# Optimization experiments

Hardware: AMD Instinct MI355X
Metric: run time of the kernel (lower is better)

## Reference

```python
import jax, jax.numpy as jnp
import numpy as np

GROUPS = 32
EPS = 1e-5


def setup_inputs() -> dict:
    key = jax.random.key(0)
    ks = jax.random.split(key, 4)
    B, C, H, W = 4, 256, 64, 64
    x = jax.random.normal(ks[0], (B, C, H, W), dtype=jnp.float32)
    gn_w = jnp.ones((C,), jnp.float32)
    gn_b = jnp.zeros((C,), jnp.float32)
    qkv_w = jax.random.normal(ks[1], (3 * C, C), dtype=jnp.float32) * (C ** -0.5)
    qkv_b = jnp.zeros((3 * C,), jnp.float32)
    proj_w = jax.random.normal(ks[2], (C, C), dtype=jnp.float32) * (C ** -0.5)
    proj_b = jnp.zeros((C,), jnp.float32)
    return {"x": x, "gn_w": gn_w, "gn_b": gn_b, "qkv_w": qkv_w,
            "qkv_b": qkv_b, "proj_w": proj_w, "proj_b": proj_b}


def _group_norm(x, w, b):
    B, C, H, W = x.shape
    xr = x.reshape(B, GROUPS, -1)                      # [B, G, (C/G)*H*W]
    mean = xr.mean(axis=-1, keepdims=True)
    var = xr.var(axis=-1, keepdims=True)               # biased, like torch
    h = ((xr - mean) * jax.lax.rsqrt(var + EPS)).reshape(B, C, H, W)
    return h * w[None, :, None, None] + b[None, :, None, None]


def reference(x, gn_w, gn_b, qkv_w, qkv_b, proj_w, proj_b):
    B, C, H, W = x.shape
    h = _group_norm(x, gn_w, gn_b)
    # 1x1 conv == channel GEMM
    qkv = jnp.einsum('oc,bchw->bohw', qkv_w, h) + qkv_b[None, :, None, None]
    qkv = qkv.reshape(B, 3, C, H * W)
    q, k, v = qkv[:, 0], qkv[:, 1], qkv[:, 2]          # [B, C, N]
    scale = C ** (-0.5)
    attn = jax.nn.softmax(jnp.einsum('bci,bcj->bij', q, k) * scale, axis=-1)
    out = jnp.einsum('bij,bcj->bci', attn, v).reshape(B, C, H, W)
    out = jnp.einsum('oc,bchw->bohw', proj_w, out) + proj_b[None, :, None, None]
    return x + out
```

## Files before the change

### kernel.cpp

```cpp
#include <hip/hip_runtime.h>
#include <hip/hip_bf16.h>
#include <math.h>

typedef __bf16 bf16;
typedef __bf16 bf16x8 __attribute__((ext_vector_type(8)));
typedef __bf16 bf16x4 __attribute__((ext_vector_type(4)));
typedef float f32x4 __attribute__((ext_vector_type(4)));
typedef float f32x16 __attribute__((ext_vector_type(16)));

#define MFMA16(a, b, c) __builtin_amdgcn_mfma_f32_16x16x32_bf16(a, b, c, 0, 0, 0)
#define MFMA32(a, b, c) __builtin_amdgcn_mfma_f32_32x32x16_bf16(a, b, c, 0, 0, 0)

#define SCALEK 0.09016844005555896f

typedef const __attribute__((address_space(1))) void* gas_t;
typedef __attribute__((address_space(3))) void* las_t;

__global__ __launch_bounds__(256) void wcvt_kernel(const float* __restrict__ qw,
                                                   bf16* __restrict__ qwb) {
  int t = blockIdx.x * 256 + threadIdx.x;
  float4 v = *(const float4*)(qw + (size_t)t * 4);
  bf16x4 o;
  o[0] = (bf16)v.x; o[1] = (bf16)v.y; o[2] = (bf16)v.z; o[3] = (bf16)v.w;
  *(bf16x4*)(qwb + (size_t)t * 4) = o;
}

__global__ __launch_bounds__(256) void gn_kernel(
    const float* __restrict__ x, const float* __restrict__ gw,
    const float* __restrict__ gb, bf16* __restrict__ h) {
  const int bg = blockIdx.x;
  const int b = bg >> 5, g = bg & 31;
  const size_t base = (size_t)(b * 256 + g * 8) * 4096;
  const float* xp = x + base;
  bf16* hp = h + base;
  const int tid = threadIdx.x;

  float s = 0.f, ss = 0.f;
  for (int i = tid * 4; i < 32768; i += 1024) {
    float4 v = *(const float4*)(xp + i);
    s += v.x + v.y + v.z + v.w;
    ss += v.x * v.x + v.y * v.y + v.z * v.z + v.w * v.w;
  }
#pragma unroll
  for (int off = 32; off; off >>= 1) {
    s += __shfl_down(s, off);
    ss += __shfl_down(ss, off);
  }
  __shared__ float red[8];
  if ((tid & 63) == 0) {
    red[(tid >> 6) * 2] = s;
    red[(tid >> 6) * 2 + 1] = ss;
  }
  __syncthreads();
  s = red[0] + red[2] + red[4] + red[6];
  ss = red[1] + red[3] + red[5] + red[7];
  const float mean = s * (1.f / 32768.f);
  const float var = ss * (1.f / 32768.f) - mean * mean;
  const float rstd = rsqrtf(var + 1e-5f);

  for (int i = tid * 4; i < 32768; i += 1024) {
    float4 v = *(const float4*)(xp + i);
    int c = g * 8 + (i >> 12);
    float a = gw[c] * rstd;
    float b2 = gb[c] - mean * a;
    bf16x4 o;
    o[0] = (bf16)(v.x * a + b2);
    o[1] = (bf16)(v.y * a + b2);
    o[2] = (bf16)(v.z * a + b2);
    o[3] = (bf16)(v.w * a + b2);
    *(bf16x4*)(hp + i) = o;
  }
}

__global__ __launch_bounds__(256) void qkv_gemm(
    const bf16* __restrict__ h, const bf16* __restrict__ wb,
    const float* __restrict__ bias, bf16* __restrict__ qt,
    bf16* __restrict__ kt, bf16* __restrict__ vcm) {
  const int b = blockIdx.z;
  const int o0 = blockIdx.y * 64;
  const int p0 = blockIdx.x * 64;
  __shared__ bf16 Alds[2][64][32];
  __shared__ bf16 Blds[2][64][56];
  const int tid = threadIdx.x;
  const int lane = tid & 63, wid = tid >> 6;
  const int lr = lane & 15, lg = lane >> 4;
  const int wm = wid >> 1, wn = wid & 1;
  const bf16* hb = h + (size_t)b * 256 * 4096;

  const int arow = tid >> 2, ac8 = (tid & 3) * 8;
  const int bcc = tid >> 3, bp8 = (tid & 7) * 8;

#define QKV_STAGE_A(K0, BUF)                                                  \
  __builtin_amdgcn_global_load_lds(                                           \
      (gas_t)(const void*)(wb + (size_t)(o0 + arow) * 256 + (K0) + ac8),      \
      (las_t)(void*)(&Alds[BUF][0][0] + tid * 8), 16, 0, 0);

  f32x4 acc[2][2] = {};

  QKV_STAGE_A(0, 0);
  {
    bf16x8 v = *(const bf16x8*)(hb + (size_t)bcc * 4096 + p0 + bp8);
#pragma unroll
    for (int e = 0; e < 8; ++e) Blds[0][bp8 + e][bcc] = v[e];
  }
  __syncthreads();

  for (int k = 0; k < 8; ++k) {
    const int cur = k & 1, nb = cur ^ 1;
    if (k < 7) {
      QKV_STAGE_A((k + 1) * 32, nb);
      bf16x8 v =
          *(const bf16x8*)(hb + (size_t)((k + 1) * 32 + bcc) * 4096 + p0 + bp8);
#pragma unroll
      for (int e = 0; e < 8; ++e) Blds[nb][bp8 + e][bcc] = v[e];
    }
    bf16x8 af[2], bfr[2];
#pragma unroll
    for (int mi = 0; mi < 2; ++mi)
      af[mi] = *(const bf16x8*)&Alds[cur][wm * 32 + mi * 16 + lr][lg * 8];
#pragma unroll
    for (int ni = 0; ni < 2; ++ni)
      bfr[ni] = *(const bf16x8*)&Blds[cur][wn * 32 + ni * 16 + lr][lg * 8];
#pragma unroll
    for (int mi = 0; mi < 2; ++mi)
#pragma unroll
      for (int ni = 0; ni < 2; ++ni)
        acc[mi][ni] = MFMA16(af[mi], bfr[ni], acc[mi][ni]);
    __syncthreads();
  }
#undef QKV_STAGE_A

#pragma unroll
  for (int mi = 0; mi < 2; ++mi) {
#pragma unroll
    for (int ni = 0; ni < 2; ++ni) {
#pragma unroll
      for (int r = 0; r < 4; ++r) {
        int o = o0 + wm * 32 + mi * 16 + lg * 4 + r;
        int p = p0 + wn * 32 + ni * 16 + lr;
        float val = acc[mi][ni][r] + bias[o];
        if (o < 256) {
          qt[((size_t)b * 4096 + p) * 256 + o] = (bf16)val;
        } else if (o < 512) {
          kt[((size_t)b * 4096 + p) * 256 + (o - 256)] = (bf16)(val * SCALEK);
        } else {
          vcm[((size_t)b * 256 + (o - 512)) * 4096 + p] = (bf16)val;
        }
      }
    }
  }
}

template <int S>
__global__ __launch_bounds__(256, 2) void flash_attn(
    const bf16* __restrict__ qt, const bf16* __restrict__ kt,
    const bf16* __restrict__ vcm, bf16* __restrict__ Opart,
    float* __restrict__ l_g) {
  constexpr int NCOMBO = 4 * S;
  constexpr int CSH = (S == 4) ? 4 : (S == 2) ? 3 : 2;
  constexpr int NIT = (4096 / S) / 32;
  const int bid = blockIdx.x;
  const int combo = bid & (NCOMBO - 1);
  const int qtile = bid >> CSH;
  const int b = combo & 3;
  const int split = combo >> 2;
  const int i0 = qtile * 128;
  const int jbase = split * (4096 / S);

  __shared__ bf16 Klds[2][32][256];
  __shared__ bf16 Vlds[2][256][32];
  const int tid = threadIdx.x;
  const int lane = tid & 63, w = tid >> 6;
  const int ln = lane & 31;
  const int hv = lane >> 5;
  const bf16* qb = qt + (size_t)b * 4096 * 256;
  const bf16* kb = kt + (size_t)b * 4096 * 256;
  const bf16* vb = vcm + (size_t)b * 256 * 4096;

  const int qrow = i0 + w * 32 + ln;
  bf16x8 qf[16];
#pragma unroll
  for (int ks = 0; ks < 16; ++ks)
    qf[ks] = *(const bf16x8*)(qb + (size_t)qrow * 256 + ks * 16 + hv * 8);

  int koff[4], voff[4];
#pragma unroll
  for (int it = 0; it < 4; ++it) {
    int chunk = tid + 256 * it;
    int krow = chunk >> 5;
    koff[it] = krow * 256 + ((((chunk & 31) ^ (krow & 7)) * 8));
    int vrow = chunk >> 2;
    voff[it] = vrow * 4096 + (((chunk & 3) ^ ((vrow >> 2) & 3)) * 8);
  }

#define STAGE_K(JT, BUF)                                                      \
  {                                                                           \
    const int j0s = jbase + (JT) * 32;                                        \
    _Pragma("unroll") for (int it = 0; it < 4; ++it) {                        \
      int chunk = tid + 256 * it;                                             \
      __builtin_amdgcn_global_load_lds(                                       \
          (gas_t)(const void*)(kb + (size_t)j0s * 256 + koff[it]),            \
          (las_t)(void*)(&Klds[BUF][0][0] + chunk * 8), 16, 0, 0);            \
    }                                                                         \
  }
#define STAGE_V(JT, BUF)                                                      \
  {                                                                           \
    const int j0s = jbase + (JT) * 32;                                        \
    _Pragma("unroll") for (int it = 0; it < 4; ++it) {                        \
      int chunk = tid + 256 * it;                                             \
      __builtin_amdgcn_global_load_lds(                                       \
          (gas_t)(const void*)(vb + (size_t)j0s + voff[it]),                  \
          (las_t)(void*)(&Vlds[BUF][0][0] + chunk * 8), 16, 0, 0);            \
    }                                                                         \
  }

  float llane = 0.f;
  f32x16 accO[8] = {};
  const int kswz = ln & 7;
  const int vswz = (ln >> 2) & 3;

  STAGE_K(0, 0);
  STAGE_V(0, 0);
  asm volatile("s_waitcnt vmcnt(0)" ::: "memory");
  __builtin_amdgcn_s_barrier();

  f32x16 a0 = {}, a1 = {};
#pragma unroll
  for (int ks = 0; ks < 8; ++ks) {
    bf16x8 kf0 = *(const bf16x8*)&Klds[0][ln][((2 * ks + hv) ^ kswz) * 8];
    bf16x8 kf1 =
        *(const bf16x8*)&Klds[0][ln][((2 * (ks + 8) + hv) ^ kswz) * 8];
    a0 = MFMA32(kf0, qf[ks], a0);
    a1 = MFMA32(kf1, qf[ks + 8], a1);
  }
  STAGE_K(1, 1);

  for (int t = 0; t < NIT; ++t) {
    asm volatile("s_waitcnt vmcnt(0)" ::: "memory");
    __builtin_amdgcn_s_barrier();

    if (t + 1 < NIT) STAGE_V(t + 1, (t + 1) & 1);
    if (t + 2 < NIT) STAGE_K(t + 2, t & 1);

    float pv[16];
#pragma unroll
    for (int r = 0; r < 16; ++r) pv[r] = exp2f(a0[r] + a1[r]);
    llane += (((pv[0] + pv[1]) + (pv[2] + pv[3])) +
              ((pv[4] + pv[5]) + (pv[6] + pv[7]))) +
             (((pv[8] + pv[9]) + (pv[10] + pv[11])) +
              ((pv[12] + pv[13]) + (pv[14] + pv[15])));

    int pk[8];
#pragma unroll
    for (int q4 = 0; q4 < 8; ++q4)
      asm("v_cvt_pk_bf16_f32 %0, %1, %2"
          : "=v"(pk[q4])
          : "v"(pv[q4 * 2]), "v"(pv[q4 * 2 + 1]));
    bf16x8 pfrag[2];
#pragma unroll
    for (int s = 0; s < 2; ++s) {
      int xa = pk[s * 4 + 0], ya = pk[s * 4 + 2];
      int xb = pk[s * 4 + 1], yb = pk[s * 4 + 3];
      asm("v_permlane32_swap_b32 %0, %1" : "+v"(xa), "+v"(ya));
      asm("v_permlane32_swap_b32 %0, %1" : "+v"(xb), "+v"(yb));
      union { int i[4]; bf16x8 v; } u;
      u.i[0] = xa; u.i[1] = xb; u.i[2] = ya; u.i[3] = yb;
      pfrag[s] = u.v;
    }

    const bf16(*Kc)[256] = Klds[(t + 1) & 1];
    const bf16(*Vc)[32] = Vlds[t & 1];
    __builtin_amdgcn_s_setprio(1);
    if (t + 1 < NIT) {
      f32x16 n0 = {}, n1 = {};
#pragma unroll
      for (int u = 0; u < 8; ++u) {
        bf16x8 kf0 = *(const bf16x8*)&Kc[ln][((2 * u + hv) ^ kswz) * 8];
        n0 = MFMA32(kf0, qf[u], n0);
        bf16x8 kf1 =
            *(const bf16x8*)&Kc[ln][((2 * (u + 8) + hv) ^ kswz) * 8];
        n1 = MFMA32(kf1, qf[u + 8], n1);
        bf16x8 vf0 = *(const bf16x8*)&Vc[u * 32 + ln][((hv) ^ vswz) * 8];
        accO[u] = MFMA32(vf0, pfrag[0], accO[u]);
        bf16x8 vf1 = *(const bf16x8*)&Vc[u * 32 + ln][((2 + hv) ^ vswz) * 8];
        accO[u] = MFMA32(vf1, pfrag[1], accO[u]);
      }
      a0 = n0;
      a1 = n1;
    } else {
#pragma unroll
      for (int u = 0; u < 8; ++u) {
        bf16x8 vf0 = *(const bf16x8*)&Vc[u * 32 + ln][((hv) ^ vswz) * 8];
        accO[u] = MFMA32(vf0, pfrag[0], accO[u]);
        bf16x8 vf1 = *(const bf16x8*)&Vc[u * 32 + ln][((2 + hv) ^ vswz) * 8];
        accO[u] = MFMA32(vf1, pfrag[1], accO[u]);
      }
    }
    __builtin_amdgcn_s_setprio(0);
  }
#undef STAGE_K
#undef STAGE_V

  bf16* ob = Opart + ((size_t)(split * 4 + b) * 4096 + qrow) * 256;
#pragma unroll
  for (int cb = 0; cb < 8; ++cb) {
#pragma unroll
    for (int g = 0; g < 4; ++g) {
      int lo, hi;
      asm("v_cvt_pk_bf16_f32 %0, %1, %2"
          : "=v"(lo)
          : "v"(accO[cb][g * 4 + 0]), "v"(accO[cb][g * 4 + 1]));
      asm("v_cvt_pk_bf16_f32 %0, %1, %2"
          : "=v"(hi)
          : "v"(accO[cb][g * 4 + 2]), "v"(accO[cb][g * 4 + 3]));
      int2 val; val.x = lo; val.y = hi;
      *(int2*)(ob + cb * 32 + g * 8 + hv * 4) = val;
    }
  }
  {
    int xa = __float_as_int(llane);
    int ya = xa;
    asm("v_permlane32_swap_b32 %0, %1" : "+v"(xa), "+v"(ya));
    float ltot = __int_as_float(xa) + __int_as_float(ya);
    if (hv == 0)
      l_g[(size_t)(split * 4 + b) * 4096 + qrow] = ltot;
  }
}

template <int S>
__global__ __launch_bounds__(256) void proj_fused(
    const bf16* __restrict__ Opart, const float* __restrict__ l_g,
    const float* __restrict__ w, const float* __restrict__ bias,
    const float* __restrict__ x, float* __restrict__ out) {
  const int b = blockIdx.y;
  const int p0 = blockIdx.x * 64;
  __shared__ bf16 Wlds[256][32];
  __shared__ bf16 Blds[64][32];
  __shared__ float Linv[64];
  const int tid = threadIdx.x;
  const int lane = tid & 63, wid = tid >> 6;
  const int lr = lane & 15, lg = lane >> 4;

  if (tid < 64) {
    float L = 0.f;
#pragma unroll
    for (int s = 0; s < S; ++s)
      L += l_g[(size_t)(s * 4 + b) * 4096 + p0 + tid];
    Linv[tid] = 1.f / L;
  }
  __syncthreads();

  const int pr = tid >> 2, c8b = (tid & 3) * 8;
  const float invp = Linv[pr];

  float4 wreg[4][2];
  bf16x8 breg[S];

#define PROJ_READ(K0)                                                         \
  {                                                                           \
    _Pragma("unroll") for (int it = 0; it < 4; ++it) {                        \
      int chunk = tid + 256 * it;                                             \
      int row = chunk >> 2, c8 = (chunk & 3) * 8;                             \
      const float* src = w + (size_t)row * 256 + (K0) + c8;                   \
      wreg[it][0] = *(const float4*)src;                                      \
      wreg[it][1] = *(const float4*)(src + 4);                                \
    }                                                                         \
    _Pragma("unroll") for (int s = 0; s < S; ++s) breg[s] =                   \
        *(const bf16x8*)(Opart +                                              \
                         ((size_t)(s * 4 + b) * 4096 + p0 + pr) * 256 +       \
                         (K0) + c8b);                                         \
  }
#define PROJ_WRITE()                                                          \
  {                                                                           \
    _Pragma("unroll") for (int it = 0; it < 4; ++it) {                        \
      int chunk = tid + 256 * it;                                             \
      int row = chunk >> 2, c8 = (chunk & 3) * 8;                             \
      bf16x8 bv;                                                              \
      bv[0] = (bf16)wreg[it][0].x; bv[1] = (bf16)wreg[it][0].y;               \
      bv[2] = (bf16)wreg[it][0].z; bv[3] = (bf16)wreg[it][0].w;               \
      bv[4] = (bf16)wreg[it][1].x; bv[5] = (bf16)wreg[it][1].y;               \
      bv[6] = (bf16)wreg[it][1].z; bv[7] = (bf16)wreg[it][1].w;               \
      *(bf16x8*)&Wlds[row][c8] = bv;                                          \
    }                                                                         \
    {                                                                         \
      float a8[8] = {};                                                       \
      _Pragma("unroll") for (int s = 0; s < S; ++s) {                         \
        _Pragma("unroll") for (int e = 0; e < 8; ++e) a8[e] +=                \
            (float)breg[s][e];                                                \
      }                                                                       \
      bf16x8 bv;                                                              \
      _Pragma("unroll") for (int e = 0; e < 8; ++e) bv[e] =                   \
          (bf16)(a8[e] * invp);                                               \
      *(bf16x8*)&Blds[pr][c8b] = bv;                                          \
    }                                                                         \
  }

  f32x4 acc[4][4] = {};

  PROJ_READ(0);
  PROJ_WRITE();
  __syncthreads();

  for (int k = 0; k < 8; ++k) {
    if (k < 7) PROJ_READ((k + 1) * 32);

    bf16x8 af[4], bfr[4];
#pragma unroll
    for (int mi = 0; mi < 4; ++mi)
      af[mi] = *(const bf16x8*)&Wlds[wid * 64 + mi * 16 + lr][lg * 8];
#pragma unroll
    for (int ni = 0; ni < 4; ++ni)
      bfr[ni] = *(const bf16x8*)&Blds[ni * 16 + lr][lg * 8];
#pragma unroll
    for (int mi = 0; mi < 4; ++mi)
#pragma unroll
      for (int ni = 0; ni < 4; ++ni)
        acc[mi][ni] = MFMA16(af[mi], bfr[ni], acc[mi][ni]);

    __syncthreads();
    if (k < 7) {
      PROJ_WRITE();
      __syncthreads();
    }
  }
#undef PROJ_READ
#undef PROJ_WRITE

#pragma unroll
  for (int mi = 0; mi < 4; ++mi) {
#pragma unroll
    for (int ni = 0; ni < 4; ++ni) {
#pragma unroll
      for (int r = 0; r < 4; ++r) {
        int o = wid * 64 + mi * 16 + lg * 4 + r;
        int p = p0 + ni * 16 + lr;
        size_t idx = ((size_t)b * 256 + o) * 4096 + p;
        out[idx] = acc[mi][ni][r] + bias[o] + x[idx];
      }
    }
  }
}

extern "C" void kernel_launch(void* const* d_in, const int* in_sizes, int n_in,
                              void* d_out, int out_size, void* d_ws,
                              size_t ws_size, hipStream_t stream) {
  (void)in_sizes; (void)n_in; (void)out_size;
  const float* x = (const float*)d_in[0];
  const float* gn_w = (const float*)d_in[1];
  const float* gn_b = (const float*)d_in[2];
  const float* qkv_w = (const float*)d_in[3];
  const float* qkv_b = (const float*)d_in[4];
  const float* proj_w = (const float*)d_in[5];
  const float* proj_b = (const float*)d_in[6];
  float* out = (float*)d_out;

  const size_t MB = 1024ull * 1024ull;
  char* ws = (char*)d_ws;
  bf16* h = (bf16*)(ws);
  bf16* qt = (bf16*)(ws + 8 * MB);
  bf16* kt = (bf16*)(ws + 16 * MB);
  bf16* vcm = (bf16*)(ws + 24 * MB);

  int S;
  if (ws_size >= 32 * MB + 4 * 8 * MB + 4ull * 16384 * sizeof(float)) S = 4;
  else if (ws_size >= 32 * MB + 2 * 8 * MB + 2ull * 16384 * sizeof(float)) S = 2;
  else S = 1;

  bf16* Opart;
  float* l_g;
  bf16* qwb;
  if (S >= 2) {
    Opart = (bf16*)(ws + 32 * MB);
    l_g = (float*)(ws + 32 * MB + (size_t)S * 8 * MB);
    qwb = Opart;
  } else {
    Opart = h;
    l_g = (float*)(ws + 32 * MB);
    qwb = (bf16*)(ws + 32 * MB + 256 * 1024);
  }

  wcvt_kernel<<<192, 256, 0, stream>>>(qkv_w, qwb);
  gn_kernel<<<128, 256, 0, stream>>>(x, gn_w, gn_b, h);
  qkv_gemm<<<dim3(64, 12, 4), 256, 0, stream>>>(h, qwb, qkv_b, qt, kt, vcm);
  if (S == 4) {
    flash_attn<4><<<32 * 16, 256, 0, stream>>>(qt, kt, vcm, Opart, l_g);
    proj_fused<4><<<dim3(64, 4), 256, 0, stream>>>(Opart, l_g, proj_w, proj_b,
                                                   x, out);
  } else if (S == 2) {
    flash_attn<2><<<32 * 8, 256, 0, stream>>>(qt, kt, vcm, Opart, l_g);
    proj_fused<2><<<dim3(64, 4), 256, 0, stream>>>(Opart, l_g, proj_w, proj_b,
                                                   x, out);
  } else {
    flash_attn<1><<<32 * 4, 256, 0, stream>>>(qt, kt, vcm, Opart, l_g);
    proj_fused<1><<<dim3(64, 4), 256, 0, stream>>>(Opart, l_g, proj_w, proj_b,
                                                   x, out);
  }
}
```

Measured before the change: 180.1 us.

## Process two query row groups per wave with 4-stage K/V pipeline

```diff
diff --git a/kernel.cpp b/kernel.cpp
--- a/kernel.cpp
+++ b/kernel.cpp
@@ -152,7 +152,7 @@
 }
 
 template <int S>
-__global__ __launch_bounds__(256, 2) void flash_attn(
+__global__ __launch_bounds__(256, 1) void flash_attn(
     const bf16* __restrict__ qt, const bf16* __restrict__ kt,
     const bf16* __restrict__ vcm, bf16* __restrict__ Opart,
     float* __restrict__ l_g) {
@@ -164,11 +164,11 @@
   const int qtile = bid >> CSH;
   const int b = combo & 3;
   const int split = combo >> 2;
-  const int i0 = qtile * 128;
+  const int i0 = qtile * 256;
   const int jbase = split * (4096 / S);
 
-  __shared__ bf16 Klds[2][32][256];
-  __shared__ bf16 Vlds[2][256][32];
+  __shared__ bf16 Klds[4][32][256];
+  __shared__ bf16 Vlds[4][256][32];
   const int tid = threadIdx.x;
   const int lane = tid & 63, w = tid >> 6;
   const int ln = lane & 31;
@@ -177,11 +177,14 @@
   const bf16* kb = kt + (size_t)b * 4096 * 256;
   const bf16* vb = vcm + (size_t)b * 256 * 4096;
 
-  const int qrow = i0 + w * 32 + ln;
-  bf16x8 qf[16];
-#pragma unroll
-  for (int ks = 0; ks < 16; ++ks)
-    qf[ks] = *(const bf16x8*)(qb + (size_t)qrow * 256 + ks * 16 + hv * 8);
+  const int qrow0 = i0 + w * 64 + ln;
+  const int qrow1 = qrow0 + 32;
+  bf16x8 qf0[16], qf1[16];
+#pragma unroll
+  for (int ks = 0; ks < 16; ++ks) {
+    qf0[ks] = *(const bf16x8*)(qb + (size_t)qrow0 * 256 + ks * 16 + hv * 8);
+    qf1[ks] = *(const bf16x8*)(qb + (size_t)qrow1 * 256 + ks * 16 + hv * 8);
+  }
 
   int koff[4], voff[4];
 #pragma unroll
@@ -193,7 +196,7 @@
     voff[it] = vrow * 4096 + (((chunk & 3) ^ ((vrow >> 2) & 3)) * 8);
   }
 
-#define STAGE_K(JT, BUF)                                                      \
+#define STAGE(JT, BUF)                                                        \
   {                                                                           \
     const int j0s = jbase + (JT) * 32;                                        \
     _Pragma("unroll") for (int it = 0; it < 4; ++it) {                        \
@@ -201,130 +204,116 @@
       __builtin_amdgcn_global_load_lds(                                       \
           (gas_t)(const void*)(kb + (size_t)j0s * 256 + koff[it]),            \
           (las_t)(void*)(&Klds[BUF][0][0] + chunk * 8), 16, 0, 0);            \
-    }                                                                         \
-  }
-#define STAGE_V(JT, BUF)                                                      \
-  {                                                                           \
-    const int j0s = jbase + (JT) * 32;                                        \
-    _Pragma("unroll") for (int it = 0; it < 4; ++it) {                        \
-      int chunk = tid + 256 * it;                                             \
       __builtin_amdgcn_global_load_lds(                                       \
           (gas_t)(const void*)(vb + (size_t)j0s + voff[it]),                  \
           (las_t)(void*)(&Vlds[BUF][0][0] + chunk * 8), 16, 0, 0);            \
     }                                                                         \
   }
 
-  float llane = 0.f;
-  f32x16 accO[8] = {};
+#define SOFTPACK(A0, A1, LL, PF)                                              \
+  {                                                                           \
+    float pv[16];                                                             \
+    _Pragma("unroll") for (int r = 0; r < 16; ++r) pv[r] =                    \
+        exp2f((A0)[r] + (A1)[r]);                                             \
+    (LL) += (((pv[0] + pv[1]) + (pv[2] + pv[3])) +                            \
+             ((pv[4] + pv[5]) + (pv[6] + pv[7]))) +                           \
+            (((pv[8] + pv[9]) + (pv[10] + pv[11])) +                          \
+             ((pv[12] + pv[13]) + (pv[14] + pv[15])));                        \
+    int pk[8];                                                                \
+    _Pragma("unroll") for (int q4 = 0; q4 < 8; ++q4)                          \
+        asm("v_cvt_pk_bf16_f32 %0, %1, %2"                                    \
+            : "=v"(pk[q4])                                                    \
+            : "v"(pv[q4 * 2]), "v"(pv[q4 * 2 + 1]));                          \
+    _Pragma("unroll") for (int s = 0; s < 2; ++s) {                           \
+      int xa = pk[s * 4 + 0], ya = pk[s * 4 + 2];                             \
+      int xb = pk[s * 4 + 1], yb = pk[s * 4 + 3];                             \
+      asm("v_permlane32_swap_b32 %0, %1" : "+v"(xa), "+v"(ya));               \
+      asm("v_permlane32_swap_b32 %0, %1" : "+v"(xb), "+v"(yb));               \
+      union { int i[4]; bf16x8 v; } u;                                        \
+      u.i[0] = xa; u.i[1] = xb; u.i[2] = ya; u.i[3] = yb;                     \
+      (PF)[s] = u.v;                                                          \
+    }                                                                         \
+  }
+
+  float ll0 = 0.f, ll1 = 0.f;
+  f32x16 acc0[8] = {}, acc1[8] = {};
   const int kswz = ln & 7;
   const int vswz = (ln >> 2) & 3;
 
-  STAGE_K(0, 0);
-  STAGE_V(0, 0);
-  asm volatile("s_waitcnt vmcnt(0)" ::: "memory");
-  __builtin_amdgcn_s_barrier();
-
-  f32x16 a0 = {}, a1 = {};
-#pragma unroll
-  for (int ks = 0; ks < 8; ++ks) {
-    bf16x8 kf0 = *(const bf16x8*)&Klds[0][ln][((2 * ks + hv) ^ kswz) * 8];
-    bf16x8 kf1 =
-        *(const bf16x8*)&Klds[0][ln][((2 * (ks + 8) + hv) ^ kswz) * 8];
-    a0 = MFMA32(kf0, qf[ks], a0);
-    a1 = MFMA32(kf1, qf[ks + 8], a1);
-  }
-  STAGE_K(1, 1);
+  STAGE(0, 0);
+  STAGE(1, 1);
+  STAGE(2, 2);
 
   for (int t = 0; t < NIT; ++t) {
-    asm volatile("s_waitcnt vmcnt(0)" ::: "memory");
+    if (t + 2 < NIT)
+      asm volatile("s_waitcnt vmcnt(16)" ::: "memory");
+    else if (t + 1 < NIT)
+      asm volatile("s_waitcnt vmcnt(8)" ::: "memory");
+    else
+      asm volatile("s_waitcnt vmcnt(0)" ::: "memory");
     __builtin_amdgcn_s_barrier();
-
-    if (t + 1 < NIT) STAGE_V(t + 1, (t + 1) & 1);
-    if (t + 2 < NIT) STAGE_K(t + 2, t & 1);
-
-    float pv[16];
-#pragma unroll
-    for (int r = 0; r < 16; ++r) pv[r] = exp2f(a0[r] + a1[r]);
-    llane += (((pv[0] + pv[1]) + (pv[2] + pv[3])) +
-              ((pv[4] + pv[5]) + (pv[6] + pv[7]))) +
-             (((pv[8] + pv[9]) + (pv[10] + pv[11])) +
-              ((pv[12] + pv[13]) + (pv[14] + pv[15])));
-
-    int pk[8];
-#pragma unroll
-    for (int q4 = 0; q4 < 8; ++q4)
-      asm("v_cvt_pk_bf16_f32 %0, %1, %2"
-          : "=v"(pk[q4])
-          : "v"(pv[q4 * 2]), "v"(pv[q4 * 2 + 1]));
-    bf16x8 pfrag[2];
-#pragma unroll
-    for (int s = 0; s < 2; ++s) {
-      int xa = pk[s * 4 + 0], ya = pk[s * 4 + 2];
-      int xb = pk[s * 4 + 1], yb = pk[s * 4 + 3];
-      asm("v_permlane32_swap_b32 %0, %1" : "+v"(xa), "+v"(ya));
-      asm("v_permlane32_swap_b32 %0, %1" : "+v"(xb), "+v"(yb));
-      union { int i[4]; bf16x8 v; } u;
-      u.i[0] = xa; u.i[1] = xb; u.i[2] = ya; u.i[3] = yb;
-      pfrag[s] = u.v;
-    }
-
-    const bf16(*Kc)[256] = Klds[(t + 1) & 1];
-    const bf16(*Vc)[32] = Vlds[t & 1];
+    if (t + 3 < NIT) STAGE(t + 3, (t + 3) & 3);
+
+    const bf16(*Kc)[256] = Klds[t & 3];
+    const bf16(*Vc)[32] = Vlds[t & 3];
+
+    f32x16 a0g0 = {}, a1g0 = {}, a0g1 = {}, a1g1 = {};
     __builtin_amdgcn_s_setprio(1);
-    if (t + 1 < NIT) {
-      f32x16 n0 = {}, n1 = {};
-#pragma unroll
-      for (int u = 0; u < 8; ++u) {
-        bf16x8 kf0 = *(const bf16x8*)&Kc[ln][((2 * u + hv) ^ kswz) * 8];
-        n0 = MFMA32(kf0, qf[u], n0);
-        bf16x8 kf1 =
-            *(const bf16x8*)&Kc[ln][((2 * (u + 8) + hv) ^ kswz) * 8];
-        n1 = MFMA32(kf1, qf[u + 8], n1);
-        bf16x8 vf0 = *(const bf16x8*)&Vc[u * 32 + ln][((hv) ^ vswz) * 8];
-        accO[u] = MFMA32(vf0, pfrag[0], accO[u]);
-        bf16x8 vf1 = *(const bf16x8*)&Vc[u * 32 + ln][((2 + hv) ^ vswz) * 8];
-        accO[u] = MFMA32(vf1, pfrag[1], accO[u]);
-      }
-      a0 = n0;
-      a1 = n1;
-    } else {
-#pragma unroll
-      for (int u = 0; u < 8; ++u) {
-        bf16x8 vf0 = *(const bf16x8*)&Vc[u * 32 + ln][((hv) ^ vswz) * 8];
-        accO[u] = MFMA32(vf0, pfrag[0], accO[u]);
-        bf16x8 vf1 = *(const bf16x8*)&Vc[u * 32 + ln][((2 + hv) ^ vswz) * 8];
-        accO[u] = MFMA32(vf1, pfrag[1], accO[u]);
-      }
+#pragma unroll
+    for (int ks = 0; ks < 8; ++ks) {
+      bf16x8 kf0 = *(const bf16x8*)&Kc[ln][((2 * ks + hv) ^ kswz) * 8];
+      bf16x8 kf1 = *(const bf16x8*)&Kc[ln][((2 * (ks + 8) + hv) ^ kswz) * 8];
+      a0g0 = MFMA32(kf0, qf0[ks], a0g0);
+      a0g1 = MFMA32(kf0, qf1[ks], a0g1);
+      a1g0 = MFMA32(kf1, qf0[ks + 8], a1g0);
+      a1g1 = MFMA32(kf1, qf1[ks + 8], a1g1);
     }
     __builtin_amdgcn_s_setprio(0);
-  }
-#undef STAGE_K
-#undef STAGE_V
-
-  bf16* ob = Opart + ((size_t)(split * 4 + b) * 4096 + qrow) * 256;
-#pragma unroll
-  for (int cb = 0; cb < 8; ++cb) {
-#pragma unroll
-    for (int g = 0; g < 4; ++g) {
-      int lo, hi;
-      asm("v_cvt_pk_bf16_f32 %0, %1, %2"
-          : "=v"(lo)
-          : "v"(accO[cb][g * 4 + 0]), "v"(accO[cb][g * 4 + 1]));
-      asm("v_cvt_pk_bf16_f32 %0, %1, %2"
-          : "=v"(hi)
-          : "v"(accO[cb][g * 4 + 2]), "v"(accO[cb][g * 4 + 3]));
-      int2 val; val.x = lo; val.y = hi;
-      *(int2*)(ob + cb * 32 + g * 8 + hv * 4) = val;
-    }
-  }
-  {
-    int xa = __float_as_int(llane);
-    int ya = xa;
-    asm("v_permlane32_swap_b32 %0, %1" : "+v"(xa), "+v"(ya));
-    float ltot = __int_as_float(xa) + __int_as_float(ya);
-    if (hv == 0)
-      l_g[(size_t)(split * 4 + b) * 4096 + qrow] = ltot;
-  }
+
+    bf16x8 pf0[2], pf1[2];
+    SOFTPACK(a0g0, a1g0, ll0, pf0);
+    SOFTPACK(a0g1, a1g1, ll1, pf1);
+
+    __builtin_amdgcn_s_setprio(1);
+#pragma unroll
+    for (int u = 0; u < 8; ++u) {
+      bf16x8 vf0 = *(const bf16x8*)&Vc[u * 32 + ln][((hv) ^ vswz) * 8];
+      bf16x8 vf1 = *(const bf16x8*)&Vc[u * 32 + ln][((2 + hv) ^ vswz) * 8];
+      acc0[u] = MFMA32(vf0, pf0[0], acc0[u]);
+      acc1[u] = MFMA32(vf0, pf1[0], acc1[u]);
+      acc0[u] = MFMA32(vf1, pf0[1], acc0[u]);
+      acc1[u] = MFMA32(vf1, pf1[1], acc1[u]);
+    }
+    __builtin_amdgcn_s_setprio(0);
+  }
+#undef STAGE
+#undef SOFTPACK
+
+#define EPI(ACC, LL, QROW)                                                    \
+  {                                                                           \
+    bf16* ob = Opart + ((size_t)(split * 4 + b) * 4096 + (QROW)) * 256;       \
+    _Pragma("unroll") for (int cb = 0; cb < 8; ++cb) {                        \
+      _Pragma("unroll") for (int g = 0; g < 4; ++g) {                         \
+        int lo, hi;                                                           \
+        asm("v_cvt_pk_bf16_f32 %0, %1, %2"                                    \
+            : "=v"(lo)                                                        \
+            : "v"((ACC)[cb][g * 4 + 0]), "v"((ACC)[cb][g * 4 + 1]));          \
+        asm("v_cvt_pk_bf16_f32 %0, %1, %2"                                    \
+            : "=v"(hi)                                                        \
+            : "v"((ACC)[cb][g * 4 + 2]), "v"((ACC)[cb][g * 4 + 3]));          \
+        int2 val; val.x = lo; val.y = hi;                                     \
+        *(int2*)(ob + cb * 32 + g * 8 + hv * 4) = val;                        \
+      }                                                                       \
+    }                                                                         \
+    int xa = __float_as_int(LL), ya = xa;                                     \
+    asm("v_permlane32_swap_b32 %0, %1" : "+v"(xa), "+v"(ya));                 \
+    float ltot = __int_as_float(xa) + __int_as_float(ya);                     \
+    if (hv == 0)                                                              \
+      l_g[(size_t)(split * 4 + b) * 4096 + (QROW)] = ltot;                    \
+  }
+  EPI(acc0, ll0, qrow0);
+  EPI(acc1, ll1, qrow1);
+#undef EPI
 }
 
 template <int S>
@@ -483,15 +472,15 @@
   gn_kernel<<<128, 256, 0, stream>>>(x, gn_w, gn_b, h);
   qkv_gemm<<<dim3(64, 12, 4), 256, 0, stream>>>(h, qwb, qkv_b, qt, kt, vcm);
   if (S == 4) {
-    flash_attn<4><<<32 * 16, 256, 0, stream>>>(qt, kt, vcm, Opart, l_g);
+    flash_attn<4><<<16 * 16, 256, 0, stream>>>(qt, kt, vcm, Opart, l_g);
     proj_fused<4><<<dim3(64, 4), 256, 0, stream>>>(Opart, l_g, proj_w, proj_b,
                                                    x, out);
   } else if (S == 2) {
-    flash_attn<2><<<32 * 8, 256, 0, stream>>>(qt, kt, vcm, Opart, l_g);
+    flash_attn<2><<<16 * 8, 256, 0, stream>>>(qt, kt, vcm, Opart, l_g);
     proj_fused<2><<<dim3(64, 4), 256, 0, stream>>>(Opart, l_g, proj_w, proj_b,
                                                    x, out);
   } else {
-    flash_attn<1><<<32 * 4, 256, 0, stream>>>(qt, kt, vcm, Opart, l_g);
+    flash_attn<1><<<16 * 4, 256, 0, stream>>>(qt, kt, vcm, Opart, l_g);
     proj_fused<1><<<dim3(64, 4), 256, 0, stream>>>(Opart, l_g, proj_w, proj_b,
                                                    x, out);
   }
```

Result: slower. 240.6 us (+33.6%).
